# Performance work log

Measured on AMD Instinct MI355X. Metric: run time of the kernel, lower is better.

The kernel has to match this reference:

```python
import jax, jax.numpy as jnp
import numpy as np

G = 16          # avg_pool_output_size (grid side after adaptive pool)
PATCH = 2       # patch_size
HIDDEN = 256
NOUT = 128


def setup_inputs() -> dict:
    key = jax.random.key(0)
    ks = jax.random.split(key, 7)
    B, C, H, W = 8, 32, 32, 32
    D = C * PATCH * PATCH + 2          # 130 (patch pixels + 2 coords)
    IN0 = 2 * D                        # 260 (pair concat)
    s = 0.02
    return {
        "x": jax.random.normal(ks[0], (B, C, H, W), jnp.float32),
        "W0": jax.random.normal(ks[1], (IN0, HIDDEN), jnp.float32) * s,
        "b0": jax.random.normal(ks[2], (HIDDEN,), jnp.float32) * s,
        "W1": jax.random.normal(ks[3], (HIDDEN, HIDDEN), jnp.float32) * s,
        "b1": jax.random.normal(ks[4], (HIDDEN,), jnp.float32) * s,
        "Wout": jax.random.normal(ks[5], (HIDDEN, NOUT), jnp.float32) * s,
        "bout": jax.random.normal(ks[6], (NOUT,), jnp.float32) * s,
    }


def _patch_node_features(x):
    """x: [B,C,H,W] -> node features [B, P, C*p^2 + 2] (patch pixels + coords)."""
    b, c, h, w = x.shape
    # adaptive avg pool to GxG (evenly divisible case == block mean)
    pooled = x.reshape(b, c, G, h // G, G, w // G).mean(axis=(3, 5))  # [B,C,G,G]
    flat = pooled.reshape(b, c, G * G)
    Pg = G - PATCH + 1                          # patches per side (15)
    P = Pg * Pg                                 # 225 nodes
    ri = jnp.arange(Pg)
    ki = jnp.arange(PATCH)
    # flat pixel index (r+ki)*G + (q+kj), patch order row-major, pixel order row-major
    row = (ri[:, None, None, None] + ki[None, None, :, None])  # [Pg,1,p,1]
    col = (ri[None, :, None, None] + ki[None, None, None, :])  # [1,Pg,1,p]
    pix = (row * G + col).reshape(P, PATCH * PATCH)            # [P, p^2]
    feats = flat[:, :, pix]                                    # [B,C,P,p^2]
    # torch: [b,c,P,p2] -> permute -> [b,c,p2,P] -> reshape [b,c*p2,P] -> [b,P,c*p2]
    feats = feats.transpose(0, 2, 1, 3).reshape(b, P, c * PATCH * PATCH)
    # spatial coordinates: (x=col, y=row) centered by int(sqrt(P)/2)
    cx = jnp.broadcast_to(jnp.arange(Pg)[None, :], (Pg, Pg))
    cy = jnp.broadcast_to(jnp.arange(Pg)[:, None], (Pg, Pg))
    coord = jnp.stack([cx, cy], axis=-1).reshape(P, 2).astype(feats.dtype) - (Pg // 2)
    coord = jnp.broadcast_to(coord[None], (b, P, 2))
    return jnp.concatenate([feats, coord], axis=2)             # [B,P,D]


def reference(x, W0, b0, W1, b1, Wout, bout):
    feats = _patch_node_features(x)          # [B,P,D]
    b, P, D = feats.shape
    # pair tensor: cat([x_i, x_j]) with x_i[b,i,j]=feats[b,j], x_j[b,i,j]=feats[b,i]
    pair = jnp.concatenate([
        jnp.broadcast_to(feats[:, None, :, :], (b, P, P, D)),
        jnp.broadcast_to(feats[:, :, None, :], (b, P, P, D)),
    ], axis=-1).reshape(b, P * P, 2 * D)     # [B, P^2, 2D]
    out = jax.nn.leaky_relu(pair @ W0 + b0)  # [B,P^2,H]
    out = jax.nn.leaky_relu(out @ W1 + b1)
    out = out.mean(axis=1)                   # [B,H]
    return out @ Wout + bout                 # [B,NOUT]
```

## Files before the change

### kernel.cpp

```cpp
#include <hip/hip_runtime.h>
#include <hip/hip_bf16.h>
#include <stdint.h>

#define NB 8
#define NP 225
#define PGRID 15
#define DH 256
#define DIN 130

typedef _Float16 f16x8 __attribute__((ext_vector_type(8)));
typedef float    f32x4 __attribute__((ext_vector_type(4)));

static __device__ __forceinline__ float lrelu(float x) { return fmaxf(x, 0.01f * x); }

__global__ void prep_kernel(const float* __restrict__ x, const float* __restrict__ W0,
                            const float* __restrict__ b0, const float* __restrict__ W1,
                            _Float16* __restrict__ U, _Float16* __restrict__ V,
                            _Float16* __restrict__ W1F, float* __restrict__ accg) {
    int blk = blockIdx.x;
    if (blk >= 360) {
        int t = (blk - 360) * 256 + threadIdx.x;
        int slot = t >> 6, l = t & 63;
        int nf = slot >> 3, ks = slot & 7;
        int n = nf * 16 + (l & 15);
        int kb = l >> 4;
        f16x8 wv;
        #pragma unroll
        for (int e = 0; e < 8; ++e) {
            int k = ks * 32 + kb * 8 + e;
            wv[e] = (_Float16)W1[k * DH + n];
        }
        reinterpret_cast<f16x8*>(W1F)[t] = wv;
        return;
    }
    int bb = blk / 45;
    int p0 = (blk % 45) * 5;
    if (blk % 45 == 0) accg[bb * DH + threadIdx.x] = 0.0f;
    __shared__ float fl[5][DIN];
    int t = threadIdx.x;
    for (int idx = t; idx < 5 * DIN; idx += 256) {
        int pp = idx / DIN, f = idx % DIN;
        int p = p0 + pp;
        int r = p / PGRID, c = p % PGRID;
        float val;
        if (f < 128) {
            int ch = f >> 2, q = f & 3, ki = q >> 1, kj = q & 1;
            int R = r + ki, C = c + kj;
            const float* xp = x + (((size_t)bb * 32 + ch) * 32 + 2 * R) * 32 + 2 * C;
            val = 0.25f * (xp[0] + xp[1] + xp[32] + xp[33]);
        } else {
            val = (f == 128) ? (float)(c - 7) : (float)(r - 7);
        }
        fl[pp][f] = val;
    }
    __syncthreads();
    int n = t;
    float u[5] = {0, 0, 0, 0, 0}, v[5] = {0, 0, 0, 0, 0};
    for (int k = 0; k < DIN; ++k) {
        float wa = W0[k * DH + n];
        float wb = W0[(DIN + k) * DH + n];
        #pragma unroll
        for (int pp = 0; pp < 5; ++pp) {
            float f = fl[pp][k];
            u[pp] = fmaf(f, wa, u[pp]);
            v[pp] = fmaf(f, wb, v[pp]);
        }
    }
    float bb0 = b0[n];
    #pragma unroll
    for (int pp = 0; pp < 5; ++pp) {
        size_t base = ((size_t)bb * NP + p0 + pp) * DH + n;
        U[base] = (_Float16)(u[pp] + bb0);
        V[base] = (_Float16)v[pp];
    }
}

__global__ __launch_bounds__(256, 2) void main_kernel(
        const _Float16* __restrict__ U, const _Float16* __restrict__ V,
        const _Float16* __restrict__ W1F, const float* __restrict__ b1,
        float* __restrict__ accg) {
    __shared__ _Float16 Upad[16 * 264];
    __shared__ _Float16 Vlds[28 * 256];
    const int JT = 15, CHUNKS = 9, TILESPC = 7;
    int blk = blockIdx.x;
    int bb = blk / (JT * CHUNKS);
    int rem = blk % (JT * CHUNKS);
    int jt = rem / CHUNKS, ch = rem % CHUNKS;
    int j0 = jt * 16;
    int tile0 = ch * TILESPC;
    int nt = min(TILESPC, 57 - tile0);
    int t = threadIdx.x, l = t & 63, w = t >> 6;

    {
        const _Float16* Vsrc = V + ((size_t)bb * NP + tile0 * 4) * DH;
        for (int q = w * 4; q < 14 && q < w * 4 + 4; ++q) {
            __builtin_amdgcn_global_load_lds(
                (const __attribute__((address_space(1))) void*)(Vsrc + q * 512 + (size_t)l * 8),
                (__attribute__((address_space(3))) void*)(&Vlds[q * 512]),
                16, 0, 0);
        }
    }
    {
        int jj = t >> 4, kk = (t & 15) * 16;
        int jc = j0 + jj; if (jc >= NP) jc = NP - 1;
        const f16x8* src = reinterpret_cast<const f16x8*>(U + ((size_t)bb * NP + jc) * DH + kk);
        *reinterpret_cast<f16x8*>(&Upad[jj * 264 + kk])     = src[0];
        *reinterpret_cast<f16x8*>(&Upad[jj * 264 + kk + 8]) = src[1];
    }
    f16x8 bv[4][8];
    const f16x8* Bp = reinterpret_cast<const f16x8*>(W1F);
    #pragma unroll
    for (int nf = 0; nf < 4; ++nf)
        #pragma unroll
        for (int ks = 0; ks < 8; ++ks)
            bv[nf][ks] = Bp[((w * 4 + nf) * 8 + ks) * 64 + l];
    float b1v[4];
    #pragma unroll
    for (int nf = 0; nf < 4; ++nf) b1v[nf] = b1[w * 64 + nf * 16 + (l & 15)];
    int rowg = l >> 4;
    float jmask[4];
    #pragma unroll
    for (int r = 0; r < 4; ++r) jmask[r] = (j0 + rowg * 4 + r) < NP ? 1.0f : 0.0f;
    float psum[4] = {0.f, 0.f, 0.f, 0.f};
    int kb = l >> 4;
    const _Float16* Urow = &Upad[(l & 15) * 264 + kb * 8];
    __syncthreads();

    for (int itl = 0; itl < nt; ++itl) {
        #pragma unroll
        for (int nf = 0; nf < 4; ++nf)
            #pragma unroll
            for (int ks = 0; ks < 8; ++ks)
                asm volatile("" : "+v"(bv[nf][ks]));

        int i0 = (tile0 + itl) * 4;
        f32x4 acc[4][4];
        #pragma unroll
        for (int mf = 0; mf < 4; ++mf)
            #pragma unroll
            for (int nf = 0; nf < 4; ++nf)
                acc[mf][nf] = (f32x4){b1v[nf], b1v[nf], b1v[nf], b1v[nf]};

        #pragma unroll
        for (int ks = 0; ks < 8; ++ks) {
            f16x8 uv = *reinterpret_cast<const f16x8*>(Urow + ks * 32);
            #pragma unroll
            for (int mf = 0; mf < 4; ++mf) {
                f16x8 vv = *reinterpret_cast<const f16x8*>(
                    &Vlds[(itl * 4 + mf) * 256 + kb * 8 + ks * 32]);
                f16x8 s = uv + vv;
                f16x8 a = __builtin_elementwise_max(s, s * (_Float16)0.01f);
                #pragma unroll
                for (int nf = 0; nf < 4; ++nf)
                    acc[mf][nf] = __builtin_amdgcn_mfma_f32_16x16x32_f16(
                        a, bv[nf][ks], acc[mf][nf], 0, 0, 0);
            }
        }

        #pragma unroll
        for (int mf = 0; mf < 4; ++mf) {
            if (i0 + mf < NP) {
                #pragma unroll
                for (int r = 0; r < 4; ++r) {
                    #pragma unroll
                    for (int nf = 0; nf < 4; ++nf) {
                        float a = acc[mf][nf][r];
                        float h = fmaxf(a, 0.01f * a);
                        psum[nf] = fmaf(h, jmask[r], psum[nf]);
                    }
                }
            }
        }
    }

    #pragma unroll
    for (int nf = 0; nf < 4; ++nf) {
        psum[nf] += __shfl_xor(psum[nf], 16);
        psum[nf] += __shfl_xor(psum[nf], 32);
    }
    if (l < 16) {
        #pragma unroll
        for (int nf = 0; nf < 4; ++nf)
            atomicAdd(&accg[bb * DH + w * 64 + nf * 16 + l], psum[nf]);
    }
}

__global__ void out_kernel(const float* __restrict__ accg, const float* __restrict__ Wout,
                           const float* __restrict__ bout, float* __restrict__ out) {
    int bb = blockIdx.x;
    int o = threadIdx.x;
    float s = 0.f;
    for (int n = 0; n < DH; ++n)
        s = fmaf(accg[bb * DH + n], Wout[n * 128 + o], s);
    out[bb * 128 + o] = s * (1.0f / 50625.0f) + bout[o];
}

extern "C" void kernel_launch(void* const* d_in, const int* in_sizes, int n_in,
                              void* d_out, int out_size, void* d_ws, size_t ws_size,
                              hipStream_t stream) {
    const float* x    = (const float*)d_in[0];
    const float* W0   = (const float*)d_in[1];
    const float* b0   = (const float*)d_in[2];
    const float* W1   = (const float*)d_in[3];
    const float* b1   = (const float*)d_in[4];
    const float* Wout = (const float*)d_in[5];
    const float* bout = (const float*)d_in[6];
    float* out = (float*)d_out;

    char* ws = (char*)d_ws;
    _Float16* U    = (_Float16*)(ws);
    _Float16* V    = (_Float16*)(ws + 921600);
    _Float16* W1F  = (_Float16*)(ws + 2 * 921600);
    float*    accg = (float*)(ws + 2 * 921600 + 131072);

    prep_kernel<<<392, 256, 0, stream>>>(x, W0, b0, W1, U, V, W1F, accg);
    main_kernel<<<NB * 15 * 9, 256, 0, stream>>>(U, V, W1F, b1, accg);
    out_kernel<<<NB, 128, 0, stream>>>(accg, Wout, bout, out);
}
```

Before: 102.0 us.

## Share pair activation tiles across waves via double-buffered LDS staging

Previously every wave recomputed the full U+V leaky-ReLU A operand for all four row fragments, so that elementwise work was done four times per block. Now each wave builds one fragment's activations and stores them to a double-buffered LDS array. All waves then read the shared tiles for their MFMAs, and the next half-tile is built while the current one is consumed. This cuts redundant VALU work but adds LDS traffic, about 32KB more shared memory, and extra block barriers per tile. It also drops the inline-asm register pinning of the B fragments, which risks changed register allocation.

After: 97.38 us. 4.6% less time.

```diff
diff --git a/kernel.cpp b/kernel.cpp
--- a/kernel.cpp
+++ b/kernel.cpp
@@ -79,6 +79,7 @@
         const _Float16* __restrict__ U, const _Float16* __restrict__ V,
         const _Float16* __restrict__ W1F, const float* __restrict__ b1,
         float* __restrict__ accg) {
+    __shared__ f16x8 Af[2][1024];
     __shared__ _Float16 Upad[16 * 264];
     __shared__ _Float16 Vlds[28 * 256];
     const int JT = 15, CHUNKS = 9, TILESPC = 7;
@@ -124,15 +125,41 @@
     float psum[4] = {0.f, 0.f, 0.f, 0.f};
     int kb = l >> 4;
     const _Float16* Urow = &Upad[(l & 15) * 264 + kb * 8];
+
+#define BUILD_HALF(ITL2, KH, BUF)                                            \
+    {                                                                        \
+        const _Float16* Vr = &Vlds[((ITL2) * 4 + w) * 256 + kb * 8];         \
+        _Pragma("unroll")                                                    \
+        for (int q = 0; q < 4; ++q) {                                        \
+            int ks_ = (KH) * 4 + q;                                          \
+            f16x8 uv = *reinterpret_cast<const f16x8*>(Urow + ks_ * 32);     \
+            f16x8 vv = *reinterpret_cast<const f16x8*>(Vr + ks_ * 32);       \
+            f16x8 s_ = uv + vv;                                              \
+            f16x8 a_ = __builtin_elementwise_max(s_, s_ * (_Float16)0.01f);  \
+            Af[BUF][(w * 4 + q) * 64 + l] = a_;                              \
+        }                                                                    \
+    }
+
+#define MFMA_HALF(KH, BUF)                                                   \
+    _Pragma("unroll")                                                        \
+    for (int ksh = 0; ksh < 4; ++ksh) {                                      \
+        f16x8 av[4];                                                         \
+        _Pragma("unroll")                                                    \
+        for (int mf = 0; mf < 4; ++mf) av[mf] = Af[BUF][(mf * 4 + ksh) * 64 + l]; \
+        _Pragma("unroll")                                                    \
+        for (int mf = 0; mf < 4; ++mf)                                       \
+            _Pragma("unroll")                                                \
+            for (int nf = 0; nf < 4; ++nf)                                   \
+                acc[mf][nf] = __builtin_amdgcn_mfma_f32_16x16x32_f16(        \
+                    av[mf], bv[nf][(KH) * 4 + ksh], acc[mf][nf], 0, 0, 0);   \
+    }
+
     __syncthreads();
+    BUILD_HALF(0, 0, 0);
+    __syncthreads();
+    int cur = 0;
 
     for (int itl = 0; itl < nt; ++itl) {
-        #pragma unroll
-        for (int nf = 0; nf < 4; ++nf)
-            #pragma unroll
-            for (int ks = 0; ks < 8; ++ks)
-                asm volatile("" : "+v"(bv[nf][ks]));
-
         int i0 = (tile0 + itl) * 4;
         f32x4 acc[4][4];
         #pragma unroll
@@ -141,21 +168,13 @@
             for (int nf = 0; nf < 4; ++nf)
                 acc[mf][nf] = (f32x4){b1v[nf], b1v[nf], b1v[nf], b1v[nf]};
 
-        #pragma unroll
-        for (int ks = 0; ks < 8; ++ks) {
-            f16x8 uv = *reinterpret_cast<const f16x8*>(Urow + ks * 32);
-            #pragma unroll
-            for (int mf = 0; mf < 4; ++mf) {
-                f16x8 vv = *reinterpret_cast<const f16x8*>(
-                    &Vlds[(itl * 4 + mf) * 256 + kb * 8 + ks * 32]);
-                f16x8 s = uv + vv;
-                f16x8 a = __builtin_elementwise_max(s, s * (_Float16)0.01f);
-                #pragma unroll
-                for (int nf = 0; nf < 4; ++nf)
-                    acc[mf][nf] = __builtin_amdgcn_mfma_f32_16x16x32_f16(
-                        a, bv[nf][ks], acc[mf][nf], 0, 0, 0);
-            }
-        }
+        BUILD_HALF(itl, 1, cur ^ 1);
+        MFMA_HALF(0, cur);
+        __syncthreads();
+        cur ^= 1;
+
+        if (itl + 1 < nt) BUILD_HALF(itl + 1, 0, cur ^ 1);
+        MFMA_HALF(1, cur);
 
         #pragma unroll
         for (int mf = 0; mf < 4; ++mf) {
@@ -171,6 +190,8 @@
                 }
             }
         }
+        __syncthreads();
+        cur ^= 1;
     }
 
     #pragma unroll
@@ -183,6 +204,8 @@
         for (int nf = 0; nf < 4; ++nf)
             atomicAdd(&accg[bb * DH + w * 64 + nf * 16 + l], psum[nf]);
     }
+#undef BUILD_HALF
+#undef MFMA_HALF
 }
 
 __global__ void out_kernel(const float* __restrict__ accg, const float* __restrict__ Wout,
```
